# Kernel tuning notes

Measured on AMD Instinct MI355X. Metric: run time of the kernel, lower is better.

The kernel has to match this reference:

```python
import jax, jax.numpy as jnp
import numpy as np
from jax import lax

N, DEG, D_IN, D_FEAT, D_HID, D_REP, G = 32768, 16, 128, 256, 256, 128, 64


def setup_inputs() -> dict:
    key = jax.random.key(0)
    ks = jax.random.split(key, 24)
    def w(k, shape):
        return (jax.random.normal(k, shape, jnp.float32) / np.sqrt(shape[0])).astype(jnp.float32)
    inp = {
        "in_feat": jax.random.normal(ks[0], (N, D_IN), jnp.float32),
        "neighbors": jax.random.randint(ks[1], (N, DEG), 0, N, jnp.int32),
        "node2graph": jnp.sort(jax.random.randint(ks[2], (N,), 0, G, jnp.int32)),
        # layer 1 (SAGEConv 128 -> 256, lstm aggregator: LSTM(128,128))
        "w_ih1": w(ks[3], (4 * D_IN, D_IN)),
        "w_hh1": w(ks[4], (4 * D_IN, D_IN)),
        "b_lstm1": jnp.zeros((4 * D_IN,), jnp.float32),
        "w_self1": w(ks[5], (D_IN, D_FEAT)),
        "w_neigh1": w(ks[6], (D_IN, D_FEAT)),
        "b1": jnp.zeros((D_FEAT,), jnp.float32),
        # layer 2 (SAGEConv 256 -> 256, LSTM(256,256))
        "w_ih2": w(ks[7], (4 * D_FEAT, D_FEAT)),
        "w_hh2": w(ks[8], (4 * D_FEAT, D_FEAT)),
        "b_lstm2": jnp.zeros((4 * D_FEAT,), jnp.float32),
        "w_self2": w(ks[9], (D_FEAT, D_HID)),
        "w_neigh2": w(ks[10], (D_FEAT, D_HID)),
        "b2": jnp.zeros((D_HID,), jnp.float32),
        # heads
        "w_mu": w(ks[11], (D_HID, D_REP)),
        "b_mu": jnp.zeros((D_REP,), jnp.float32),
        "w_sigma": w(ks[12], (D_HID, D_REP)),
        "b_sigma": jnp.zeros((D_REP,), jnp.float32),
    }
    return inp


def _lstm_agg(seq, w_ih, w_hh, b):
    # seq: [N, L, D] neighbor messages; LSTM with zero init, return final hidden h.
    n, _, d = seq.shape
    h0 = jnp.zeros((n, d), seq.dtype)
    def step(carry, x):
        h, c = carry
        gates = x @ w_ih.T + h @ w_hh.T + b  # [N, 4D]
        i, f, g, o = jnp.split(gates, 4, axis=-1)  # pytorch gate order i,f,g,o
        c = jax.nn.sigmoid(f) * c + jax.nn.sigmoid(i) * jnp.tanh(g)
        h = jax.nn.sigmoid(o) * jnp.tanh(c)
        return (h, c), None
    (h, _), _ = lax.scan(step, (h0, h0), jnp.swapaxes(seq, 0, 1))
    return h


def _sage_lstm(feat, neighbors, w_ih, w_hh, b_lstm, w_self, w_neigh, b):
    msgs = feat[neighbors]                      # irregular gather [N, DEG, D]
    h_n = _lstm_agg(msgs, w_ih, w_hh, b_lstm)   # [N, D]
    return feat @ w_self + h_n @ w_neigh + b


def reference(in_feat, neighbors, node2graph,
              w_ih1, w_hh1, b_lstm1, w_self1, w_neigh1, b1,
              w_ih2, w_hh2, b_lstm2, w_self2, w_neigh2, b2,
              w_mu, b_mu, w_sigma, b_sigma):
    h = _sage_lstm(in_feat, neighbors, w_ih1, w_hh1, b_lstm1, w_self1, w_neigh1, b1)
    h = jax.nn.relu(h)
    h = _sage_lstm(h, neighbors, w_ih2, w_hh2, b_lstm2, w_self2, w_neigh2, b2)
    # dgl.mean_nodes: per-graph mean over nodes
    sums = jax.ops.segment_sum(h, node2graph, num_segments=G)
    cnts = jax.ops.segment_sum(jnp.ones((h.shape[0],), h.dtype), node2graph, num_segments=G)
    x = sums / jnp.maximum(cnts, 1.0)[:, None]
    return (x @ w_mu + b_mu, x @ w_sigma + b_sigma)
```

## Files before the change

### kernel.cpp

```cpp
#include <hip/hip_runtime.h>
#include <hip/hip_bf16.h>
#include <cstddef>

#define NN_   32768
#define DEG_  16
#define D1_   128
#define D2_   256
#define G_    64
#define DREP_ 128

typedef __attribute__((ext_vector_type(8))) short bf16x8;
typedef __attribute__((ext_vector_type(4))) float f32x4;
typedef __attribute__((ext_vector_type(4))) unsigned short us4;
typedef unsigned short ushort_t;

__device__ __attribute__((aligned(16))) ushort_t g_feat1[(size_t)NN_ * D1_];
__device__ __attribute__((aligned(16))) ushort_t g_hfeat[(size_t)NN_ * D2_];
__device__ __attribute__((aligned(16))) ushort_t g_hA[(size_t)NN_ * D2_];
__device__ __attribute__((aligned(16))) ushort_t g_hB[(size_t)NN_ * D2_];
__device__ __attribute__((aligned(16))) ushort_t g_c[(size_t)NN_ * D2_];
__device__ __attribute__((aligned(16))) ushort_t g_P[(size_t)NN_ * 1024];
__device__ __attribute__((aligned(16))) float    g_outh[(size_t)NN_ * D2_];
__device__ __attribute__((aligned(16))) ushort_t g_wih1[512 * 128];
__device__ __attribute__((aligned(16))) ushort_t g_whh1[512 * 128];
__device__ __attribute__((aligned(16))) ushort_t g_wself1[256 * 128];
__device__ __attribute__((aligned(16))) ushort_t g_wneigh1[256 * 128];
__device__ __attribute__((aligned(16))) ushort_t g_wih2[1024 * 256];
__device__ __attribute__((aligned(16))) ushort_t g_whh2[1024 * 256];
__device__ __attribute__((aligned(16))) ushort_t g_wself2[256 * 256];
__device__ __attribute__((aligned(16))) ushort_t g_wneigh2[256 * 256];
__device__ float g_gsum[G_ * D2_];
__device__ int   g_gcnt[G_];

__device__ __forceinline__ ushort_t f2bf(float f) {
    unsigned int u = __float_as_uint(f);
    u += 0x7fffu + ((u >> 16) & 1u);
    return (ushort_t)(u >> 16);
}
__device__ __forceinline__ float bf2f(ushort_t u) {
    return __uint_as_float(((unsigned int)u) << 16);
}
__device__ __forceinline__ float sigf(float x) { return 1.f / (1.f + __expf(-x)); }
__device__ __forceinline__ float tanhf_(float x) { return 1.f - 2.f / (__expf(2.f * x) + 1.f); }

__global__ __launch_bounds__(256) void cvt_bf16(const float* __restrict__ src,
                                                ushort_t* __restrict__ dst, int n)
{
    int i = blockIdx.x * 256 + threadIdx.x;
    if (i < n) dst[i] = f2bf(src[i]);
}

__global__ __launch_bounds__(256) void cvt_bf16_T(const float* __restrict__ src,
                                                  ushort_t* __restrict__ dst, int K, int N)
{
    int i = blockIdx.x * 256 + threadIdx.x;
    if (i < K * N) {
        int k = i / N, n = i % N;
        dst[n * K + k] = f2bf(src[i]);
    }
}

template<bool DUAL, bool HAS_BIAS, bool RELU, bool OUTBF>
__global__ __launch_bounds__(256) void gemm_mfma(
    const ushort_t* __restrict__ A1, const ushort_t* __restrict__ B1,
    const ushort_t* __restrict__ A2, const ushort_t* __restrict__ B2,
    const float* __restrict__ bias, float* __restrict__ Cf,
    ushort_t* __restrict__ Cb, int M, int N, int K)
{
    __shared__ ushort_t As[64][72];
    __shared__ ushort_t Bs[64][72];
    const int tid = threadIdx.x;
    const int l = tid & 63, w = tid >> 6;
    const int m0 = blockIdx.y * 64, n0 = blockIdx.x * 64;

    f32x4 acc[4];
#pragma unroll
    for (int m = 0; m < 4; ++m) acc[m] = (f32x4){0.f, 0.f, 0.f, 0.f};

    const int npass = DUAL ? 2 : 1;
    for (int pass = 0; pass < npass; ++pass) {
        const ushort_t* __restrict__ A = (DUAL && pass) ? A2 : A1;
        const ushort_t* __restrict__ B = (DUAL && pass) ? B2 : B1;
        for (int k0 = 0; k0 < K; k0 += 64) {
#pragma unroll
            for (int i = 0; i < 2; ++i) {
                int cid = tid + 256 * i;
                int row = cid >> 3, col = (cid & 7) * 8;
                *(uint4*)&As[row][col] = *(const uint4*)&A[(size_t)(m0 + row) * K + k0 + col];
                *(uint4*)&Bs[row][col] = *(const uint4*)&B[(size_t)(n0 + row) * K + k0 + col];
            }
            __syncthreads();
#pragma unroll
            for (int kk = 0; kk < 64; kk += 32) {
                bf16x8 b = *(const bf16x8*)&Bs[16 * w + (l & 15)][kk + (l >> 4) * 8];
#pragma unroll
                for (int m = 0; m < 4; ++m) {
                    bf16x8 a = *(const bf16x8*)&As[16 * m + (l & 15)][kk + (l >> 4) * 8];
                    acc[m] = __builtin_amdgcn_mfma_f32_16x16x32_bf16(a, b, acc[m], 0, 0, 0);
                }
            }
            __syncthreads();
        }
    }

#pragma unroll
    for (int m = 0; m < 4; ++m) {
#pragma unroll
        for (int r = 0; r < 4; ++r) {
            int row = m0 + 16 * m + (l >> 4) * 4 + r;
            int col = n0 + 16 * w + (l & 15);
            float v = acc[m][r];
            if (HAS_BIAS) v += bias[col];
            if (RELU) v = fmaxf(v, 0.f);
            if (OUTBF) Cb[(size_t)row * N + col] = f2bf(v);
            else       Cf[(size_t)row * N + col] = v;
        }
    }
}

template<int D>
__global__ __launch_bounds__(256) void lstm_step2(
    const ushort_t* __restrict__ h_prev, const ushort_t* __restrict__ whh,
    const ushort_t* __restrict__ P, const int* __restrict__ nbr,
    ushort_t* __restrict__ c, ushort_t* __restrict__ h_next, int t)
{
    constexpr int HP = D + 8;
    constexpr int KC = D / 32;
    __shared__ ushort_t As[64][HP];

    const int tid = threadIdx.x;
    const int l = tid & 63, w = tid >> 6;
    const int lr = l & 15, lg = l >> 4;
    const int m0 = blockIdx.x * 64;
    const int d0 = blockIdx.y * 64;
    const int dd = d0 + w * 16 + lg * 4;

    constexpr int CH = 64 * D / 8;
#pragma unroll
    for (int cid = tid; cid < CH; cid += 256) {
        int row = cid / (D / 8), cc = (cid % (D / 8)) * 8;
        *(uint4*)&As[row][cc] = *(const uint4*)&h_prev[(size_t)(m0 + row) * D + cc];
    }

    int js[4];
#pragma unroll
    for (int nt = 0; nt < 4; ++nt)
        js[nt] = nbr[(size_t)(m0 + nt * 16 + lr) * DEG_ + t];

    us4 pg[4][4];
    us4 cold[4];
#pragma unroll
    for (int nt = 0; nt < 4; ++nt) {
        size_t base = (size_t)js[nt] * (4 * D) + dd;
#pragma unroll
        for (int g = 0; g < 4; ++g)
            pg[nt][g] = *(const us4*)&P[base + g * D];
        cold[nt] = *(const us4*)&c[(size_t)(m0 + nt * 16 + lr) * D + dd];
    }

    f32x4 acc[4][4];
#pragma unroll
    for (int g = 0; g < 4; ++g)
#pragma unroll
        for (int nt = 0; nt < 4; ++nt) acc[g][nt] = (f32x4){0.f, 0.f, 0.f, 0.f};

    __syncthreads();

#pragma unroll
    for (int kc = 0; kc < KC; ++kc) {
        const int k0 = kc * 32;
        bf16x8 a[4];
#pragma unroll
        for (int g = 0; g < 4; ++g)
            a[g] = *(const bf16x8*)&whh[(size_t)(g * D + d0 + w * 16 + lr) * D + k0 + lg * 8];
        bf16x8 b[4];
#pragma unroll
        for (int nt = 0; nt < 4; ++nt)
            b[nt] = *(const bf16x8*)&As[nt * 16 + lr][k0 + lg * 8];
#pragma unroll
        for (int g = 0; g < 4; ++g)
#pragma unroll
            for (int nt = 0; nt < 4; ++nt)
                acc[g][nt] = __builtin_amdgcn_mfma_f32_16x16x32_bf16(a[g], b[nt], acc[g][nt], 0, 0, 0);
    }

#pragma unroll
    for (int nt = 0; nt < 4; ++nt) {
        us4 cnew, hnew;
#pragma unroll
        for (int r = 0; r < 4; ++r) {
            float gi = acc[0][nt][r] + bf2f(pg[nt][0][r]);
            float gf = acc[1][nt][r] + bf2f(pg[nt][1][r]);
            float gg = acc[2][nt][r] + bf2f(pg[nt][2][r]);
            float go = acc[3][nt][r] + bf2f(pg[nt][3][r]);
            float cn = sigf(gf) * bf2f(cold[nt][r]) + sigf(gi) * tanhf_(gg);
            cnew[r] = f2bf(cn);
            hnew[r] = f2bf(sigf(go) * tanhf_(cn));
        }
        size_t ci = (size_t)(m0 + nt * 16 + lr) * D + dd;
        *(us4*)&c[ci] = cnew;
        *(us4*)&h_next[ci] = hnew;
    }
}

template<int D>
__global__ __launch_bounds__(256) void cell_first(
    const ushort_t* __restrict__ P, const int* __restrict__ nbr,
    ushort_t* __restrict__ c, ushort_t* __restrict__ h_out)
{
    int idx = blockIdx.x * 256 + threadIdx.x;
    int n = idx / D, d = idx % D;
    int j = nbr[n * DEG_];
    size_t base = (size_t)j * (4 * D);
    float gi = bf2f(P[base + d]);
    float gg = bf2f(P[base + 2 * D + d]);
    float go = bf2f(P[base + 3 * D + d]);
    float cn = sigf(gi) * tanhf_(gg);
    c[idx] = f2bf(cn);
    h_out[idx] = f2bf(sigf(go) * tanhf_(cn));
}

__global__ void graph_counts(const int* __restrict__ n2g, int* __restrict__ cnt)
{
    __shared__ int lb[G_ + 1];
    int g = threadIdx.x;
    if (g <= G_) {
        int lo = 0, hi = NN_;
        while (lo < hi) {
            int mid = (lo + hi) >> 1;
            if (n2g[mid] < g) lo = mid + 1; else hi = mid;
        }
        lb[g] = lo;
    }
    __syncthreads();
    if (g < G_) cnt[g] = lb[g + 1] - lb[g];
}

__global__ __launch_bounds__(256) void seg_sum(
    const float* __restrict__ X, const int* __restrict__ n2g,
    float* __restrict__ gsum)
{
    int d = threadIdx.x;
    int n_start = blockIdx.x * 64;
    int cur = n2g[n_start];
    float acc = 0.f;
    for (int n = n_start; n < n_start + 64; ++n) {
        int g = n2g[n];
        if (g != cur) {
            atomicAdd(&gsum[cur * D2_ + d], acc);
            acc = 0.f;
            cur = g;
        }
        acc += X[(size_t)n * D2_ + d];
    }
    atomicAdd(&gsum[cur * D2_ + d], acc);
}

__global__ __launch_bounds__(128) void head_kernel(
    const float* __restrict__ gsum, const int* __restrict__ cnt,
    const float* __restrict__ w_mu, const float* __restrict__ b_mu,
    const float* __restrict__ w_sig, const float* __restrict__ b_sig,
    float* __restrict__ out)
{
    __shared__ float x[D2_];
    int g = blockIdx.x, j = threadIdx.x;
    float inv = 1.f / fmaxf((float)cnt[g], 1.f);
    x[j] = gsum[g * D2_ + j] * inv;
    x[j + 128] = gsum[g * D2_ + 128 + j] * inv;
    __syncthreads();
    float mu = b_mu[j], sg = b_sig[j];
    for (int k = 0; k < D2_; ++k) {
        float xv = x[k];
        mu += xv * w_mu[k * DREP_ + j];
        sg += xv * w_sig[k * DREP_ + j];
    }
    out[g * DREP_ + j] = mu;
    out[G_ * DREP_ + g * DREP_ + j] = sg;
}

extern "C" void kernel_launch(void* const* d_in, const int* in_sizes, int n_in,
                              void* d_out, int out_size, void* d_ws, size_t ws_size,
                              hipStream_t stream)
{
    const float* in_feat   = (const float*)d_in[0];
    const int*   neighbors = (const int*)d_in[1];
    const int*   node2graph= (const int*)d_in[2];
    const float* w_ih1     = (const float*)d_in[3];
    const float* w_hh1     = (const float*)d_in[4];
    const float* b_lstm1   = (const float*)d_in[5];
    const float* w_self1   = (const float*)d_in[6];
    const float* w_neigh1  = (const float*)d_in[7];
    const float* b1        = (const float*)d_in[8];
    const float* w_ih2     = (const float*)d_in[9];
    const float* w_hh2     = (const float*)d_in[10];
    const float* b_lstm2   = (const float*)d_in[11];
    const float* w_self2   = (const float*)d_in[12];
    const float* w_neigh2  = (const float*)d_in[13];
    const float* b2        = (const float*)d_in[14];
    const float* w_mu      = (const float*)d_in[15];
    const float* b_mu      = (const float*)d_in[16];
    const float* w_sigma   = (const float*)d_in[17];
    const float* b_sigma   = (const float*)d_in[18];

    void *pF1, *pHF, *pHA, *pHB, *pC, *pP, *pOH;
    void *pWI1, *pWH1, *pWS1, *pWN1, *pWI2, *pWH2, *pWS2, *pWN2, *pGS, *pGC;
    hipGetSymbolAddress(&pF1, HIP_SYMBOL(g_feat1));
    hipGetSymbolAddress(&pHF, HIP_SYMBOL(g_hfeat));
    hipGetSymbolAddress(&pHA, HIP_SYMBOL(g_hA));
    hipGetSymbolAddress(&pHB, HIP_SYMBOL(g_hB));
    hipGetSymbolAddress(&pC,  HIP_SYMBOL(g_c));
    hipGetSymbolAddress(&pP,  HIP_SYMBOL(g_P));
    hipGetSymbolAddress(&pOH, HIP_SYMBOL(g_outh));
    hipGetSymbolAddress(&pWI1, HIP_SYMBOL(g_wih1));
    hipGetSymbolAddress(&pWH1, HIP_SYMBOL(g_whh1));
    hipGetSymbolAddress(&pWS1, HIP_SYMBOL(g_wself1));
    hipGetSymbolAddress(&pWN1, HIP_SYMBOL(g_wneigh1));
    hipGetSymbolAddress(&pWI2, HIP_SYMBOL(g_wih2));
    hipGetSymbolAddress(&pWH2, HIP_SYMBOL(g_whh2));
    hipGetSymbolAddress(&pWS2, HIP_SYMBOL(g_wself2));
    hipGetSymbolAddress(&pWN2, HIP_SYMBOL(g_wneigh2));
    hipGetSymbolAddress(&pGS, HIP_SYMBOL(g_gsum));
    hipGetSymbolAddress(&pGC, HIP_SYMBOL(g_gcnt));

    ushort_t* feat1 = (ushort_t*)pF1;
    ushort_t* hfeat = (ushort_t*)pHF;
    ushort_t* hA    = (ushort_t*)pHA;
    ushort_t* hB    = (ushort_t*)pHB;
    ushort_t* c     = (ushort_t*)pC;
    ushort_t* P     = (ushort_t*)pP;
    float*    outh  = (float*)pOH;
    ushort_t* wih1  = (ushort_t*)pWI1;
    ushort_t* whh1  = (ushort_t*)pWH1;
    ushort_t* wself1= (ushort_t*)pWS1;
    ushort_t* wneigh1=(ushort_t*)pWN1;
    ushort_t* wih2  = (ushort_t*)pWI2;
    ushort_t* whh2  = (ushort_t*)pWH2;
    ushort_t* wself2= (ushort_t*)pWS2;
    ushort_t* wneigh2=(ushort_t*)pWN2;
    float*    gsum  = (float*)pGS;
    int*      gcnt  = (int*)pGC;

    cvt_bf16<<<(NN_ * D1_ + 255) / 256, 256, 0, stream>>>(in_feat, feat1, NN_ * D1_);
    cvt_bf16<<<(512 * 128 + 255) / 256, 256, 0, stream>>>(w_ih1, wih1, 512 * 128);
    cvt_bf16<<<(512 * 128 + 255) / 256, 256, 0, stream>>>(w_hh1, whh1, 512 * 128);
    cvt_bf16_T<<<(128 * 256 + 255) / 256, 256, 0, stream>>>(w_self1, wself1, 128, 256);
    cvt_bf16_T<<<(128 * 256 + 255) / 256, 256, 0, stream>>>(w_neigh1, wneigh1, 128, 256);
    cvt_bf16<<<(1024 * 256 + 255) / 256, 256, 0, stream>>>(w_ih2, wih2, 1024 * 256);
    cvt_bf16<<<(1024 * 256 + 255) / 256, 256, 0, stream>>>(w_hh2, whh2, 1024 * 256);
    cvt_bf16_T<<<(256 * 256 + 255) / 256, 256, 0, stream>>>(w_self2, wself2, 256, 256);
    cvt_bf16_T<<<(256 * 256 + 255) / 256, 256, 0, stream>>>(w_neigh2, wneigh2, 256, 256);

    gemm_mfma<false, true, false, true>
        <<<dim3(512 / 64, NN_ / 64), 256, 0, stream>>>(
            feat1, wih1, nullptr, nullptr, b_lstm1, nullptr, P, NN_, 512, D1_);

    cell_first<D1_><<<(NN_ * D1_) / 256, 256, 0, stream>>>(P, neighbors, c, hA);
    for (int t = 1; t < DEG_; ++t) {
        const ushort_t* hp = (t & 1) ? hA : hB;
        ushort_t*       hn = (t & 1) ? hB : hA;
        lstm_step2<D1_><<<dim3(NN_ / 64, D1_ / 64), 256, 0, stream>>>(
            hp, whh1, P, neighbors, c, hn, t);
    }

    gemm_mfma<true, true, true, true>
        <<<dim3(256 / 64, NN_ / 64), 256, 0, stream>>>(
            feat1, wself1, hB, wneigh1, b1, nullptr, hfeat, NN_, D2_, D1_);

    gemm_mfma<false, true, false, true>
        <<<dim3(1024 / 64, NN_ / 64), 256, 0, stream>>>(
            hfeat, wih2, nullptr, nullptr, b_lstm2, nullptr, P, NN_, 1024, D2_);

    cell_first<D2_><<<(NN_ * D2_) / 256, 256, 0, stream>>>(P, neighbors, c, hA);
    for (int t = 1; t < DEG_; ++t) {
        const ushort_t* hp = (t & 1) ? hA : hB;
        ushort_t*       hn = (t & 1) ? hB : hA;
        lstm_step2<D2_><<<dim3(NN_ / 64, D2_ / 64), 256, 0, stream>>>(
            hp, whh2, P, neighbors, c, hn, t);
    }

    gemm_mfma<true, true, false, false>
        <<<dim3(256 / 64, NN_ / 64), 256, 0, stream>>>(
            hfeat, wself2, hB, wneigh2, b2, outh, nullptr, NN_, D2_, D2_);

    hipMemsetAsync(gsum, 0, (size_t)G_ * D2_ * sizeof(float), stream);
    graph_counts<<<1, 128, 0, stream>>>(node2graph, gcnt);
    seg_sum<<<NN_ / 64, 256, 0, stream>>>(outh, node2graph, gsum);
    head_kernel<<<G_, 128, 0, stream>>>(gsum, gcnt, w_mu, b_mu, w_sigma, b_sigma,
                                        (float*)d_out);
}
```

Baseline: 1.811 ms.

## Fuse all LSTM timesteps into one persistent kernel with LDS-resident state

Replaces the per-timestep launch loop (cell_first plus 15 lstm_step2 launches per layer) with a single kernel per layer. Each block owns 32 nodes and keeps h (double-buffered) and c in LDS across all 16 timesteps. This removes the per-step kernel launches and the global round trips for h and c. In exchange, each block re-reads the whole w_hh matrix from global/L2 on every step, and each block covers fewer nodes, so MFMA reuse of the weights per load drops.

```diff
diff --git a/kernel.cpp b/kernel.cpp
--- a/kernel.cpp
+++ b/kernel.cpp
@@ -16,9 +16,7 @@
 
 __device__ __attribute__((aligned(16))) ushort_t g_feat1[(size_t)NN_ * D1_];
 __device__ __attribute__((aligned(16))) ushort_t g_hfeat[(size_t)NN_ * D2_];
-__device__ __attribute__((aligned(16))) ushort_t g_hA[(size_t)NN_ * D2_];
 __device__ __attribute__((aligned(16))) ushort_t g_hB[(size_t)NN_ * D2_];
-__device__ __attribute__((aligned(16))) ushort_t g_c[(size_t)NN_ * D2_];
 __device__ __attribute__((aligned(16))) ushort_t g_P[(size_t)NN_ * 1024];
 __device__ __attribute__((aligned(16))) float    g_outh[(size_t)NN_ * D2_];
 __device__ __attribute__((aligned(16))) ushort_t g_wih1[512 * 128];
@@ -119,105 +117,107 @@
 }
 
 template<int D>
-__global__ __launch_bounds__(256) void lstm_step2(
-    const ushort_t* __restrict__ h_prev, const ushort_t* __restrict__ whh,
-    const ushort_t* __restrict__ P, const int* __restrict__ nbr,
-    ushort_t* __restrict__ c, ushort_t* __restrict__ h_next, int t)
+__global__ __launch_bounds__(256, 3) void lstm_persist2(
+    const ushort_t* __restrict__ whh,
+    const ushort_t* __restrict__ P,
+    const int* __restrict__ nbr,
+    ushort_t* __restrict__ h_out)
 {
     constexpr int HP = D + 8;
     constexpr int KC = D / 32;
-    __shared__ ushort_t As[64][HP];
+    constexpr int NU = D / 64;
+    __shared__ ushort_t h_lds[2][32][HP];
+    __shared__ ushort_t c_lds[32][HP];
+    __shared__ int      nbr_lds[32][DEG_];
 
     const int tid = threadIdx.x;
     const int l = tid & 63, w = tid >> 6;
     const int lr = l & 15, lg = l >> 4;
-    const int m0 = blockIdx.x * 64;
-    const int d0 = blockIdx.y * 64;
-    const int dd = d0 + w * 16 + lg * 4;
-
-    constexpr int CH = 64 * D / 8;
+    const int n0 = blockIdx.x * 32;
+
+    for (int i = tid; i < 32 * DEG_; i += 256)
+        nbr_lds[i >> 4][i & 15] = nbr[(size_t)(n0 + (i >> 4)) * DEG_ + (i & 15)];
+    __syncthreads();
+
+    for (int t = 0; t < DEG_; ++t) {
+        const int rb = t & 1, wb = rb ^ 1;
+
+#pragma unroll
+        for (int u = 0; u < NU; ++u) {
+            const int d0 = u * 64;
+            const int dd = d0 + w * 16 + lg * 4;
+
+            int js[2];
+#pragma unroll
+            for (int nt = 0; nt < 2; ++nt)
+                js[nt] = nbr_lds[nt * 16 + lr][t];
+
+            us4 pg[2][4];
+#pragma unroll
+            for (int nt = 0; nt < 2; ++nt) {
+                size_t base = (size_t)js[nt] * (4 * D) + dd;
+#pragma unroll
+                for (int g = 0; g < 4; ++g)
+                    pg[nt][g] = *(const us4*)&P[base + g * D];
+            }
+
+            f32x4 acc[4][2];
+#pragma unroll
+            for (int g = 0; g < 4; ++g)
+#pragma unroll
+                for (int nt = 0; nt < 2; ++nt) acc[g][nt] = (f32x4){0.f, 0.f, 0.f, 0.f};
+
+            if (t > 0) {
+#pragma unroll
+                for (int kc = 0; kc < KC; ++kc) {
+                    const int k0 = kc * 32;
+                    bf16x8 a[4];
+#pragma unroll
+                    for (int g = 0; g < 4; ++g)
+                        a[g] = *(const bf16x8*)&whh[(size_t)(g * D + d0 + w * 16 + lr) * D + k0 + lg * 8];
+                    bf16x8 b[2];
+#pragma unroll
+                    for (int nt = 0; nt < 2; ++nt)
+                        b[nt] = *(const bf16x8*)&h_lds[rb][nt * 16 + lr][k0 + lg * 8];
+#pragma unroll
+                    for (int g = 0; g < 4; ++g)
+#pragma unroll
+                        for (int nt = 0; nt < 2; ++nt)
+                            acc[g][nt] = __builtin_amdgcn_mfma_f32_16x16x32_bf16(
+                                a[g], b[nt], acc[g][nt], 0, 0, 0);
+                }
+            }
+
+#pragma unroll
+            for (int nt = 0; nt < 2; ++nt) {
+                const int node = nt * 16 + lr;
+                us4 cold = (t > 0) ? *(const us4*)&c_lds[node][dd]
+                                   : (us4){0, 0, 0, 0};
+                us4 cnew, hnew;
+#pragma unroll
+                for (int r = 0; r < 4; ++r) {
+                    float gi = acc[0][nt][r] + bf2f(pg[nt][0][r]);
+                    float gf = acc[1][nt][r] + bf2f(pg[nt][1][r]);
+                    float gg = acc[2][nt][r] + bf2f(pg[nt][2][r]);
+                    float go = acc[3][nt][r] + bf2f(pg[nt][3][r]);
+                    float cp = (t > 0) ? bf2f(cold[r]) : 0.f;
+                    float cn = sigf(gf) * cp + sigf(gi) * tanhf_(gg);
+                    cnew[r] = f2bf(cn);
+                    hnew[r] = f2bf(sigf(go) * tanhf_(cn));
+                }
+                *(us4*)&c_lds[node][dd] = cnew;
+                *(us4*)&h_lds[wb][node][dd] = hnew;
+            }
+        }
+        __syncthreads();
+    }
+
+    constexpr int CH = 32 * D / 8;
 #pragma unroll
     for (int cid = tid; cid < CH; cid += 256) {
         int row = cid / (D / 8), cc = (cid % (D / 8)) * 8;
-        *(uint4*)&As[row][cc] = *(const uint4*)&h_prev[(size_t)(m0 + row) * D + cc];
-    }
-
-    int js[4];
-#pragma unroll
-    for (int nt = 0; nt < 4; ++nt)
-        js[nt] = nbr[(size_t)(m0 + nt * 16 + lr) * DEG_ + t];
-
-    us4 pg[4][4];
-    us4 cold[4];
-#pragma unroll
-    for (int nt = 0; nt < 4; ++nt) {
-        size_t base = (size_t)js[nt] * (4 * D) + dd;
-#pragma unroll
-        for (int g = 0; g < 4; ++g)
-            pg[nt][g] = *(const us4*)&P[base + g * D];
-        cold[nt] = *(const us4*)&c[(size_t)(m0 + nt * 16 + lr) * D + dd];
-    }
-
-    f32x4 acc[4][4];
-#pragma unroll
-    for (int g = 0; g < 4; ++g)
-#pragma unroll
-        for (int nt = 0; nt < 4; ++nt) acc[g][nt] = (f32x4){0.f, 0.f, 0.f, 0.f};
-
-    __syncthreads();
-
-#pragma unroll
-    for (int kc = 0; kc < KC; ++kc) {
-        const int k0 = kc * 32;
-        bf16x8 a[4];
-#pragma unroll
-        for (int g = 0; g < 4; ++g)
-            a[g] = *(const bf16x8*)&whh[(size_t)(g * D + d0 + w * 16 + lr) * D + k0 + lg * 8];
-        bf16x8 b[4];
-#pragma unroll
-        for (int nt = 0; nt < 4; ++nt)
-            b[nt] = *(const bf16x8*)&As[nt * 16 + lr][k0 + lg * 8];
-#pragma unroll
-        for (int g = 0; g < 4; ++g)
-#pragma unroll
-            for (int nt = 0; nt < 4; ++nt)
-                acc[g][nt] = __builtin_amdgcn_mfma_f32_16x16x32_bf16(a[g], b[nt], acc[g][nt], 0, 0, 0);
-    }
-
-#pragma unroll
-    for (int nt = 0; nt < 4; ++nt) {
-        us4 cnew, hnew;
-#pragma unroll
-        for (int r = 0; r < 4; ++r) {
-            float gi = acc[0][nt][r] + bf2f(pg[nt][0][r]);
-            float gf = acc[1][nt][r] + bf2f(pg[nt][1][r]);
-            float gg = acc[2][nt][r] + bf2f(pg[nt][2][r]);
-            float go = acc[3][nt][r] + bf2f(pg[nt][3][r]);
-            float cn = sigf(gf) * bf2f(cold[nt][r]) + sigf(gi) * tanhf_(gg);
-            cnew[r] = f2bf(cn);
-            hnew[r] = f2bf(sigf(go) * tanhf_(cn));
-        }
-        size_t ci = (size_t)(m0 + nt * 16 + lr) * D + dd;
-        *(us4*)&c[ci] = cnew;
-        *(us4*)&h_next[ci] = hnew;
-    }
-}
-
-template<int D>
-__global__ __launch_bounds__(256) void cell_first(
-    const ushort_t* __restrict__ P, const int* __restrict__ nbr,
-    ushort_t* __restrict__ c, ushort_t* __restrict__ h_out)
-{
-    int idx = blockIdx.x * 256 + threadIdx.x;
-    int n = idx / D, d = idx % D;
-    int j = nbr[n * DEG_];
-    size_t base = (size_t)j * (4 * D);
-    float gi = bf2f(P[base + d]);
-    float gg = bf2f(P[base + 2 * D + d]);
-    float go = bf2f(P[base + 3 * D + d]);
-    float cn = sigf(gi) * tanhf_(gg);
-    c[idx] = f2bf(cn);
-    h_out[idx] = f2bf(sigf(go) * tanhf_(cn));
+        *(bf16x8*)&h_out[(size_t)(n0 + row) * D + cc] = *(const bf16x8*)&h_lds[0][row][cc];
+    }
 }
 
 __global__ void graph_counts(const int* __restrict__ n2g, int* __restrict__ cnt)
@@ -302,13 +302,11 @@
     const float* w_sigma   = (const float*)d_in[17];
     const float* b_sigma   = (const float*)d_in[18];
 
-    void *pF1, *pHF, *pHA, *pHB, *pC, *pP, *pOH;
+    void *pF1, *pHF, *pHB, *pP, *pOH;
     void *pWI1, *pWH1, *pWS1, *pWN1, *pWI2, *pWH2, *pWS2, *pWN2, *pGS, *pGC;
     hipGetSymbolAddress(&pF1, HIP_SYMBOL(g_feat1));
     hipGetSymbolAddress(&pHF, HIP_SYMBOL(g_hfeat));
-    hipGetSymbolAddress(&pHA, HIP_SYMBOL(g_hA));
     hipGetSymbolAddress(&pHB, HIP_SYMBOL(g_hB));
-    hipGetSymbolAddress(&pC,  HIP_SYMBOL(g_c));
     hipGetSymbolAddress(&pP,  HIP_SYMBOL(g_P));
     hipGetSymbolAddress(&pOH, HIP_SYMBOL(g_outh));
     hipGetSymbolAddress(&pWI1, HIP_SYMBOL(g_wih1));
@@ -324,9 +322,7 @@
 
     ushort_t* feat1 = (ushort_t*)pF1;
     ushort_t* hfeat = (ushort_t*)pHF;
-    ushort_t* hA    = (ushort_t*)pHA;
     ushort_t* hB    = (ushort_t*)pHB;
-    ushort_t* c     = (ushort_t*)pC;
     ushort_t* P     = (ushort_t*)pP;
     float*    outh  = (float*)pOH;
     ushort_t* wih1  = (ushort_t*)pWI1;
@@ -354,13 +350,7 @@
         <<<dim3(512 / 64, NN_ / 64), 256, 0, stream>>>(
             feat1, wih1, nullptr, nullptr, b_lstm1, nullptr, P, NN_, 512, D1_);
 
-    cell_first<D1_><<<(NN_ * D1_) / 256, 256, 0, stream>>>(P, neighbors, c, hA);
-    for (int t = 1; t < DEG_; ++t) {
-        const ushort_t* hp = (t & 1) ? hA : hB;
-        ushort_t*       hn = (t & 1) ? hB : hA;
-        lstm_step2<D1_><<<dim3(NN_ / 64, D1_ / 64), 256, 0, stream>>>(
-            hp, whh1, P, neighbors, c, hn, t);
-    }
+    lstm_persist2<D1_><<<NN_ / 32, 256, 0, stream>>>(whh1, P, neighbors, hB);
 
     gemm_mfma<true, true, true, true>
         <<<dim3(256 / 64, NN_ / 64), 256, 0, stream>>>(
@@ -370,13 +360,7 @@
         <<<dim3(1024 / 64, NN_ / 64), 256, 0, stream>>>(
             hfeat, wih2, nullptr, nullptr, b_lstm2, nullptr, P, NN_, 1024, D2_);
 
-    cell_first<D2_><<<(NN_ * D2_) / 256, 256, 0, stream>>>(P, neighbors, c, hA);
-    for (int t = 1; t < DEG_; ++t) {
-        const ushort_t* hp = (t & 1) ? hA : hB;
-        ushort_t*       hn = (t & 1) ? hB : hA;
-        lstm_step2<D2_><<<dim3(NN_ / 64, D2_ / 64), 256, 0, stream>>>(
-            hp, whh2, P, neighbors, c, hn, t);
-    }
+    lstm_persist2<D2_><<<NN_ / 32, 256, 0, stream>>>(whh2, P, neighbors, hB);
 
     gemm_mfma<true, true, false, false>
         <<<dim3(256 / 64, NN_ / 64), 256, 0, stream>>>(
```

Result: slower. 2.879 ms (+59.0%).

## Double node tile in LSTM step kernel and prefetch recurrent weights

Applied to the files above, without the earlier changes.

The per-timestep LSTM kernel now handles 128 nodes per block instead of 64, so each recurrent-weight fragment loaded from global memory feeds twice as many MFMAs. The weight fragments for the next K chunk are software-prefetched into registers, and the gathered P and old cell-state loads move after the matmul rather than being issued up front. This adds LDS (about 66KB for D=256) and doubles accumulator registers, and launch_bounds(256,2) may cause spills. Latency of the gather is no longer hidden behind the GEMM.

```diff
diff --git a/kernel.cpp b/kernel.cpp
--- a/kernel.cpp
+++ b/kernel.cpp
@@ -119,85 +119,88 @@
 }
 
 template<int D>
-__global__ __launch_bounds__(256) void lstm_step2(
+__global__ __launch_bounds__(256, 2) void lstm_step3(
     const ushort_t* __restrict__ h_prev, const ushort_t* __restrict__ whh,
     const ushort_t* __restrict__ P, const int* __restrict__ nbr,
     ushort_t* __restrict__ c, ushort_t* __restrict__ h_next, int t)
 {
     constexpr int HP = D + 8;
     constexpr int KC = D / 32;
-    __shared__ ushort_t As[64][HP];
+    constexpr int NT = 8;
+    __shared__ ushort_t As[128][HP];
 
     const int tid = threadIdx.x;
     const int l = tid & 63, w = tid >> 6;
     const int lr = l & 15, lg = l >> 4;
-    const int m0 = blockIdx.x * 64;
+    const int m0 = blockIdx.x * 128;
     const int d0 = blockIdx.y * 64;
     const int dd = d0 + w * 16 + lg * 4;
 
-    constexpr int CH = 64 * D / 8;
+    constexpr int CH = 128 * D / 8;
 #pragma unroll
     for (int cid = tid; cid < CH; cid += 256) {
         int row = cid / (D / 8), cc = (cid % (D / 8)) * 8;
         *(uint4*)&As[row][cc] = *(const uint4*)&h_prev[(size_t)(m0 + row) * D + cc];
     }
 
-    int js[4];
-#pragma unroll
-    for (int nt = 0; nt < 4; ++nt)
-        js[nt] = nbr[(size_t)(m0 + nt * 16 + lr) * DEG_ + t];
-
-    us4 pg[4][4];
-    us4 cold[4];
-#pragma unroll
-    for (int nt = 0; nt < 4; ++nt) {
-        size_t base = (size_t)js[nt] * (4 * D) + dd;
+    f32x4 acc[4][NT];
+#pragma unroll
+    for (int g = 0; g < 4; ++g)
+#pragma unroll
+        for (int nt = 0; nt < NT; ++nt) acc[g][nt] = (f32x4){0.f, 0.f, 0.f, 0.f};
+
+    __syncthreads();
+
+    const ushort_t* __restrict__ wbase = &whh[(size_t)(d0 + w * 16 + lr) * D + lg * 8];
+    bf16x8 a_cur[4], a_nxt[4];
+#pragma unroll
+    for (int g = 0; g < 4; ++g)
+        a_cur[g] = *(const bf16x8*)&wbase[(size_t)g * D * D];
+
+#pragma unroll
+    for (int kc = 0; kc < KC; ++kc) {
+        if (kc + 1 < KC) {
+#pragma unroll
+            for (int g = 0; g < 4; ++g)
+                a_nxt[g] = *(const bf16x8*)&wbase[(size_t)g * D * D + (kc + 1) * 32];
+        }
+        bf16x8 b[NT];
+#pragma unroll
+        for (int nt = 0; nt < NT; ++nt)
+            b[nt] = *(const bf16x8*)&As[nt * 16 + lr][kc * 32 + lg * 8];
 #pragma unroll
         for (int g = 0; g < 4; ++g)
-            pg[nt][g] = *(const us4*)&P[base + g * D];
-        cold[nt] = *(const us4*)&c[(size_t)(m0 + nt * 16 + lr) * D + dd];
-    }
-
-    f32x4 acc[4][4];
-#pragma unroll
-    for (int g = 0; g < 4; ++g)
-#pragma unroll
-        for (int nt = 0; nt < 4; ++nt) acc[g][nt] = (f32x4){0.f, 0.f, 0.f, 0.f};
-
-    __syncthreads();
-
-#pragma unroll
-    for (int kc = 0; kc < KC; ++kc) {
-        const int k0 = kc * 32;
-        bf16x8 a[4];
+#pragma unroll
+            for (int nt = 0; nt < NT; ++nt)
+                acc[g][nt] = __builtin_amdgcn_mfma_f32_16x16x32_bf16(
+                    a_cur[g], b[nt], acc[g][nt], 0, 0, 0);
+#pragma unroll
+        for (int g = 0; g < 4; ++g) a_cur[g] = a_nxt[g];
+    }
+
+#pragma unroll
+    for (int nt = 0; nt < NT; ++nt) {
+        const int node = m0 + nt * 16 + lr;
+        const int j = nbr[(size_t)node * DEG_ + t];
+        const size_t base = (size_t)j * (4 * D) + dd;
+        us4 pg[4];
 #pragma unroll
         for (int g = 0; g < 4; ++g)
-            a[g] = *(const bf16x8*)&whh[(size_t)(g * D + d0 + w * 16 + lr) * D + k0 + lg * 8];
-        bf16x8 b[4];
-#pragma unroll
-        for (int nt = 0; nt < 4; ++nt)
-            b[nt] = *(const bf16x8*)&As[nt * 16 + lr][k0 + lg * 8];
-#pragma unroll
-        for (int g = 0; g < 4; ++g)
-#pragma unroll
-            for (int nt = 0; nt < 4; ++nt)
-                acc[g][nt] = __builtin_amdgcn_mfma_f32_16x16x32_bf16(a[g], b[nt], acc[g][nt], 0, 0, 0);
-    }
-
-#pragma unroll
-    for (int nt = 0; nt < 4; ++nt) {
+            pg[g] = *(const us4*)&P[base + g * D];
+        const size_t ci = (size_t)node * D + dd;
+        us4 cold = *(const us4*)&c[ci];
+
         us4 cnew, hnew;
 #pragma unroll
         for (int r = 0; r < 4; ++r) {
-            float gi = acc[0][nt][r] + bf2f(pg[nt][0][r]);
-            float gf = acc[1][nt][r] + bf2f(pg[nt][1][r]);
-            float gg = acc[2][nt][r] + bf2f(pg[nt][2][r]);
-            float go = acc[3][nt][r] + bf2f(pg[nt][3][r]);
-            float cn = sigf(gf) * bf2f(cold[nt][r]) + sigf(gi) * tanhf_(gg);
+            float gi = acc[0][nt][r] + bf2f(pg[0][r]);
+            float gf = acc[1][nt][r] + bf2f(pg[1][r]);
+            float gg = acc[2][nt][r] + bf2f(pg[2][r]);
+            float go = acc[3][nt][r] + bf2f(pg[3][r]);
+            float cn = sigf(gf) * bf2f(cold[r]) + sigf(gi) * tanhf_(gg);
             cnew[r] = f2bf(cn);
             hnew[r] = f2bf(sigf(go) * tanhf_(cn));
         }
-        size_t ci = (size_t)(m0 + nt * 16 + lr) * D + dd;
         *(us4*)&c[ci] = cnew;
         *(us4*)&h_next[ci] = hnew;
     }
@@ -358,7 +361,7 @@
     for (int t = 1; t < DEG_; ++t) {
         const ushort_t* hp = (t & 1) ? hA : hB;
         ushort_t*       hn = (t & 1) ? hB : hA;
-        lstm_step2<D1_><<<dim3(NN_ / 64, D1_ / 64), 256, 0, stream>>>(
+        lstm_step3<D1_><<<dim3(NN_ / 128, D1_ / 64), 256, 0, stream>>>(
             hp, whh1, P, neighbors, c, hn, t);
     }
 
@@ -374,7 +377,7 @@
     for (int t = 1; t < DEG_; ++t) {
         const ushort_t* hp = (t & 1) ? hA : hB;
         ushort_t*       hn = (t & 1) ? hB : hA;
-        lstm_step2<D2_><<<dim3(NN_ / 64, D2_ / 64), 256, 0, stream>>>(
+        lstm_step3<D2_><<<dim3(NN_ / 128, D2_ / 64), 256, 0, stream>>>(
             hp, whh2, P, neighbors, c, hn, t);
     }
 
```

After: 1.465 ms. 19.1% less time.
